# Performance work log

Measured on AMD Instinct MI355X. Metric: run time of the kernel, lower is better.

Reference implementation:

```python
import jax, jax.numpy as jnp
import numpy as np

K = 32          # neighbors
EPS = 1e-8


def _knn_gather(x, k):
    """x: [B,N,3] -> neighbors [B,N,k,3] via cdist + top-k (irregular gather)."""
    sq = jnp.sum(x * x, axis=-1)                                   # [B,N]
    # squared pairwise distances  [B,N,N]
    d = sq[:, :, None] + sq[:, None, :] - 2.0 * jnp.einsum('bnd,bmd->bnm', x, x)
    _, idx = jax.lax.top_k(-d, k)                                  # [B,N,k] nearest (incl. self)
    nbrs = jax.vmap(lambda pts, ind: pts[ind])(x, idx)             # [B,N,k,3]
    return nbrs


def _gpc2(x, k, lv):
    """Geometric point grouping: per-point 15 (or 30 with LV) channel features."""
    nbrs = _knn_gather(x, k)                                       # [B,N,k,3]
    rel = nbrs - x[:, :, None, :]                                  # relative offsets
    mu = jnp.mean(rel, axis=2)                                     # Laplace vector [B,N,3]
    r_max = jnp.max(rel, axis=2)
    r_min = jnp.min(rel, axis=2)
    r_std = jnp.std(rel, axis=2)
    feats = [x, mu, r_max, r_min, r_std]
    if lv:
        unit_mu = mu / (jnp.linalg.norm(mu, axis=-1, keepdims=True) + EPS)
        feats += [x - mu,
                  unit_mu,
                  jnp.cross(x, unit_mu),
                  jnp.max(rel * rel, axis=2),
                  jnp.mean(rel * rel, axis=2)]                     # +15 -> 30 channels
    return jnp.concatenate(feats, axis=-1)                         # [B,N,inc]


def setup_inputs() -> dict:
    key = jax.random.key(0)
    kx, kw = jax.random.split(key)
    B, N, emb, inc = 16, 4096, 32, 30
    x = jax.random.normal(kx, (B, N, 3), dtype=jnp.float32)
    W = jax.random.normal(kw, (emb, inc), dtype=jnp.float32) * 0.1
    b = jnp.zeros((emb,), dtype=jnp.float32)
    return {"x": x, "W": W, "b": b}


def reference(x, W, b):
    in_f = _gpc2(x, K, lv=True)                                    # [B,N,30]
    pooled = jnp.max(in_f, axis=1)                                 # [B,30] global max-pool
    return pooled @ W.T + b                                        # [B,32]
```

## Files before the change

### kernel.cpp

```cpp
#include <hip/hip_runtime.h>

#pragma clang fp contract(off)

#define BATCH 16
#define NPTS  4096
#define KNN   32
#define CH    30
#define NW    8
#define CHUNK (NPTS / NW)
#define FD    30
#define FSTR  31

#define INF_F __builtin_inff()

__device__ __forceinline__ unsigned enc_f32(float f) {
    unsigned u = __float_as_uint(f);
    return (u & 0x80000000u) ? ~u : (u | 0x80000000u);
}
__device__ __forceinline__ float dec_f32(unsigned e) {
    unsigned u = (e & 0x80000000u) ? (e & 0x7FFFFFFFu) : ~e;
    return __uint_as_float(u);
}

__device__ __forceinline__ float med3f(float a, float b, float c) {
#if __has_builtin(__builtin_amdgcn_fmed3f)
    return __builtin_amdgcn_fmed3f(a, b, c);
#else
    float r;
    asm("v_med3_f32 %0, %1, %2, %3" : "=v"(r) : "v"(a), "v"(b), "v"(c));
    return r;
#endif
}

__device__ __forceinline__ float dist3d(float qx, float qy, float qz,
                                        float px, float py, float pz) {
    float r0 = px - qx, r1 = py - qy, r2 = pz - qz;
    return __builtin_fmaf(r0, r0, __builtin_fmaf(r1, r1, r2 * r2));
}

__global__ void init_pool_kernel(unsigned* __restrict__ pool) {
    int i = blockIdx.x * blockDim.x + threadIdx.x;
    if (i < BATCH * CH) pool[i] = 0u;
}

__launch_bounds__(512, 8)
__global__ void knn_kernel(const float* __restrict__ x,
                           unsigned* __restrict__ pool) {
    __shared__ unsigned short fifo[NW * 64 * FSTR];
    __shared__ float scratch[CH * 64];
    __shared__ unsigned char cbs[NW * 64];

    const int b   = blockIdx.x >> 6;
    const int qg  = blockIdx.x & 63;
    const int tid = threadIdx.x;
    const int w   = tid >> 6;
    const int l   = tid & 63;
    const int q   = qg * 64 + l;
    const float* __restrict__ xb = x + (size_t)b * NPTS * 3;

    const float qx = xb[q * 3 + 0], qy = xb[q * 3 + 1], qz = xb[q * 3 + 2];

    const int wu = __builtin_amdgcn_readfirstlane(w);
    const float* __restrict__ cw = xb + (size_t)wu * (CHUNK * 3);

    float B0 = INF_F, B1 = INF_F, B2 = INF_F, B3 = INF_F;
#define INSERT4(dv)                          \
    {                                        \
        B3 = med3f(B2, B3, (dv));            \
        B2 = med3f(B1, B2, (dv));            \
        B1 = med3f(B0, B1, (dv));            \
        B0 = fminf(B0, (dv));                \
    }
#pragma unroll 4
    for (int m = 0; m < CHUNK; ++m) {
        float px = cw[3 * m + 0], py = cw[3 * m + 1], pz = cw[3 * m + 2];
        float d = dist3d(qx, qy, qz, px, py, pz);
        INSERT4(d);
    }
#undef INSERT4
    scratch[w * 64 + l] = B3;
    __syncthreads();
    float t_cap = scratch[l];
#pragma unroll
    for (int ww = 1; ww < NW; ++ww) t_cap = fmaxf(t_cap, scratch[ww * 64 + l]);

    unsigned short* __restrict__ fl = fifo + (w * 64 + l) * FSTR;
    int cnt = 0;
#pragma unroll 4
    for (int m = 0; m < CHUNK; ++m) {
        float px = cw[3 * m + 0], py = cw[3 * m + 1], pz = cw[3 * m + 2];
        float d = dist3d(qx, qy, qz, px, py, pz);
        bool t = (d <= t_cap) && (cnt < FD);
        fl[t ? cnt : FD] = (unsigned short)(wu * CHUNK + m);
        cnt += t;
    }
    cbs[w * 64 + l] = (unsigned char)cnt;
    __syncthreads();

    float* __restrict__ feat = scratch;

#define BSTEP(V, K, J)                                            \
    {                                                             \
        float pv_ = __shfl_xor((V), (J), 64);                     \
        bool km_ = (((l & (K)) == 0) == ((l & (J)) == 0));        \
        (V) = km_ ? fminf((V), pv_) : fmaxf((V), pv_);            \
    }
#define SORT64(V)                                                      \
    BSTEP(V, 2, 1)                                                     \
    BSTEP(V, 4, 2)  BSTEP(V, 4, 1)                                     \
    BSTEP(V, 8, 4)  BSTEP(V, 8, 2)  BSTEP(V, 8, 1)                     \
    BSTEP(V, 16, 8) BSTEP(V, 16, 4) BSTEP(V, 16, 2) BSTEP(V, 16, 1)    \
    BSTEP(V, 32,16) BSTEP(V, 32, 8) BSTEP(V, 32, 4) BSTEP(V, 32, 2) BSTEP(V, 32, 1) \
    BSTEP(V, 64,32) BSTEP(V, 64,16) BSTEP(V, 64, 8) BSTEP(V, 64, 4) BSTEP(V, 64, 2) BSTEP(V, 64, 1)
#define CLEAN64(V) \
    BSTEP(V, 64,32) BSTEP(V, 64,16) BSTEP(V, 64, 8) BSTEP(V, 64, 4) BSTEP(V, 64, 2) BSTEP(V, 64, 1)

#define SURV_LOAD(OFF, DOR, PX, PY, PZ)                                       \
    {                                                                         \
        int o_ = (OFF) + l;                                                   \
        int base_ = 0;                                                        \
        base_ = (o_ >= P1) ? P1 : base_;  base_ = (o_ >= P2) ? P2 : base_;    \
        base_ = (o_ >= P3) ? P3 : base_;  base_ = (o_ >= P4) ? P4 : base_;    \
        base_ = (o_ >= P5) ? P5 : base_;  base_ = (o_ >= P6) ? P6 : base_;    \
        base_ = (o_ >= P7) ? P7 : base_;                                      \
        int reg_ = (o_>=P1)+(o_>=P2)+(o_>=P3)+(o_>=P4)+(o_>=P5)+(o_>=P6)+(o_>=P7); \
        int s_ = o_ - base_;  s_ = (s_ > FD) ? FD : s_;                       \
        int idx_ = (int)fifo[(reg_ * 64 + j) * FSTR + s_];                    \
        const float* pp_ = xb + 3 * idx_;                                     \
        (PX) = pp_[0]; (PY) = pp_[1]; (PZ) = pp_[2];                          \
        float d_ = dist3d(qjx, qjy, qjz, (PX), (PY), (PZ));                   \
        (DOR) = (o_ < S) ? d_ : INF_F;                                        \
    }

#define RSUM(V) { _Pragma("unroll") for (int o_ = 32; o_ >= 1; o_ >>= 1) (V) += __shfl_xor((V), o_, 64); }
#define RMAXW(V) { _Pragma("unroll") for (int o_ = 32; o_ >= 1; o_ >>= 1) (V) = fmaxf((V), __shfl_xor((V), o_, 64)); }
#define RMINW(V) { _Pragma("unroll") for (int o_ = 32; o_ >= 1; o_ >>= 1) (V) = fminf((V), __shfl_xor((V), o_, 64)); }

#pragma unroll 1
    for (int jj = 0; jj < 8; ++jj) {
        const int j  = w * 8 + jj;
        const int qj = qg * 64 + j;
        const float qjx = xb[qj * 3 + 0], qjy = xb[qj * 3 + 1], qjz = xb[qj * 3 + 2];

        const int c0 = cbs[0 * 64 + j], c1 = cbs[1 * 64 + j],
                  c2 = cbs[2 * 64 + j], c3 = cbs[3 * 64 + j],
                  c4 = cbs[4 * 64 + j], c5 = cbs[5 * 64 + j],
                  c6 = cbs[6 * 64 + j], c7 = cbs[7 * 64 + j];
        const int P1 = c0,      P2 = P1 + c1, P3 = P2 + c2, P4 = P3 + c3,
                  P5 = P4 + c4, P6 = P5 + c5, P7 = P6 + c6, S  = P7 + c7;

        float px1, py1, pz1, dor1;
        SURV_LOAD(0, dor1, px1, py1, pz1);
        float v = dor1;
        SORT64(v)

        float thr;
        float px2 = 0.f, py2 = 0.f, pz2 = 0.f, dor2 = INF_F;
        const bool two = (S > 64);
        if (two) {
            SURV_LOAD(64, dor2, px2, py2, pz2);
            float v2 = dor2;
            SORT64(v2)
            float rb = __shfl(v2, 63 - l, 64);
            float lo = fminf(v, rb);
            CLEAN64(lo)
            thr = __shfl(lo, 31, 64);
        } else {
            thr = __shfl(v, 31, 64);
        }

        const unsigned long long blt = (l == 0) ? 0ull : (~0ull >> (64 - l));
        unsigned long long meq1 = __ballot(dor1 == thr);
        int clt = __popcll(__ballot(dor1 < thr));
        int neq1 = __popcll(meq1);
        int rank1 = __popcll(meq1 & blt);
        int rank2 = 0;
        if (two) {
            unsigned long long meq2 = __ballot(dor2 == thr);
            clt += __popcll(__ballot(dor2 < thr));
            rank2 = neq1 + __popcll(meq2 & blt);
        }
        const int need = KNN - clt;
        const bool take1 = (dor1 < thr) || ((dor1 == thr) && (rank1 < need));
        const bool take2 = two && ((dor2 < thr) || ((dor2 == thr) && (rank2 < need)));

        float r10 = px1 - qjx, r11 = py1 - qjy, r12 = pz1 - qjz;
        float r20 = px2 - qjx, r21 = py2 - qjy, r22 = pz2 - qjz;
        float s0 = (take1 ? r10 : 0.f) + (take2 ? r20 : 0.f);
        float s1 = (take1 ? r11 : 0.f) + (take2 ? r21 : 0.f);
        float s2 = (take1 ? r12 : 0.f) + (take2 ? r22 : 0.f);
        float ss0 = (take1 ? r10 * r10 : 0.f) + (take2 ? r20 * r20 : 0.f);
        float ss1 = (take1 ? r11 * r11 : 0.f) + (take2 ? r21 * r21 : 0.f);
        float ss2 = (take1 ? r12 * r12 : 0.f) + (take2 ? r22 * r22 : 0.f);
        float mx0 = fmaxf(take1 ? r10 : -INF_F, take2 ? r20 : -INF_F);
        float mx1 = fmaxf(take1 ? r11 : -INF_F, take2 ? r21 : -INF_F);
        float mx2 = fmaxf(take1 ? r12 : -INF_F, take2 ? r22 : -INF_F);
        float mn0 = fminf(take1 ? r10 : INF_F, take2 ? r20 : INF_F);
        float mn1 = fminf(take1 ? r11 : INF_F, take2 ? r21 : INF_F);
        float mn2 = fminf(take1 ? r12 : INF_F, take2 ? r22 : INF_F);

        RSUM(s0)  RSUM(s1)  RSUM(s2)
        RSUM(ss0) RSUM(ss1) RSUM(ss2)
        RMAXW(mx0) RMAXW(mx1) RMAXW(mx2)
        RMINW(mn0) RMINW(mn1) RMINW(mn2)

        const float invk = 1.0f / (float)KNN;
        float mu0 = s0 * invk, mu1 = s1 * invk, mu2 = s2 * invk;
        float ex0 = ss0 * invk, ex1 = ss1 * invk, ex2 = ss2 * invk;
        float st0 = sqrtf(fmaxf(ex0 - mu0 * mu0, 0.f));
        float st1 = sqrtf(fmaxf(ex1 - mu1 * mu1, 0.f));
        float st2 = sqrtf(fmaxf(ex2 - mu2 * mu2, 0.f));
        float nrm = sqrtf(mu0 * mu0 + mu1 * mu1 + mu2 * mu2) + 1e-8f;
        float u0 = mu0 / nrm, u1 = mu1 / nrm, u2 = mu2 / nrm;
        float cr0 = qjy * u2 - qjz * u1;
        float cr1 = qjz * u0 - qjx * u2;
        float cr2 = qjx * u1 - qjy * u0;
        float mq0 = fmaxf(mx0 * mx0, mn0 * mn0);
        float mq1 = fmaxf(mx1 * mx1, mn1 * mn1);
        float mq2 = fmaxf(mx2 * mx2, mn2 * mn2);

        if (l == 0) {
            feat[ 0 * 64 + j] = qjx;        feat[ 1 * 64 + j] = qjy;
            feat[ 2 * 64 + j] = qjz;        feat[ 3 * 64 + j] = mu0;
            feat[ 4 * 64 + j] = mu1;        feat[ 5 * 64 + j] = mu2;
            feat[ 6 * 64 + j] = mx0;        feat[ 7 * 64 + j] = mx1;
            feat[ 8 * 64 + j] = mx2;        feat[ 9 * 64 + j] = mn0;
            feat[10 * 64 + j] = mn1;        feat[11 * 64 + j] = mn2;
            feat[12 * 64 + j] = st0;        feat[13 * 64 + j] = st1;
            feat[14 * 64 + j] = st2;        feat[15 * 64 + j] = qjx - mu0;
            feat[16 * 64 + j] = qjy - mu1;  feat[17 * 64 + j] = qjz - mu2;
            feat[18 * 64 + j] = u0;         feat[19 * 64 + j] = u1;
            feat[20 * 64 + j] = u2;         feat[21 * 64 + j] = cr0;
            feat[22 * 64 + j] = cr1;        feat[23 * 64 + j] = cr2;
            feat[24 * 64 + j] = mq0;        feat[25 * 64 + j] = mq1;
            feat[26 * 64 + j] = mq2;        feat[27 * 64 + j] = ex0;
            feat[28 * 64 + j] = ex1;        feat[29 * 64 + j] = ex2;
        }
    }
    __syncthreads();

    if (w == 0) {
        for (int c = 0; c < CH; ++c) {
            float v_ = feat[c * 64 + l];
            RMAXW(v_)
            if (l == 0) atomicMax(pool + b * CH + c, enc_f32(v_));
        }
    }
#undef BSTEP
#undef SORT64
#undef CLEAN64
#undef SURV_LOAD
#undef RSUM
#undef RMAXW
#undef RMINW
}

__global__ void final_mm_kernel(const unsigned* __restrict__ pool,
                                const float* __restrict__ W,
                                const float* __restrict__ bias,
                                float* __restrict__ out) {
    int t = blockIdx.x * blockDim.x + threadIdx.x;
    if (t >= BATCH * 32) return;
    int bb = t >> 5, e = t & 31;
    float acc = bias[e];
#pragma unroll
    for (int c = 0; c < CH; ++c)
        acc += dec_f32(pool[bb * CH + c]) * W[e * CH + c];
    out[bb * 32 + e] = acc;
}

extern "C" void kernel_launch(void* const* d_in, const int* in_sizes, int n_in,
                              void* d_out, int out_size, void* d_ws, size_t ws_size,
                              hipStream_t stream) {
    const float* x    = (const float*)d_in[0];
    const float* W    = (const float*)d_in[1];
    const float* bias = (const float*)d_in[2];
    float*       out  = (float*)d_out;
    unsigned*    pool = (unsigned*)d_ws;

    hipLaunchKernelGGL(init_pool_kernel, dim3(1), dim3(512), 0, stream, pool);
    hipLaunchKernelGGL(knn_kernel, dim3(BATCH * (NPTS / 64)), dim3(512),
                       0, stream, x, pool);
    hipLaunchKernelGGL(final_mm_kernel, dim3(1), dim3(512), 0, stream, pool, W, bias, out);
}
```

Measured before the change: 203.7 us.

## Stage candidate points through LDS in two halves for KNN scans

Each block now copies its batch's points into shared memory in two 2048-point halves with float4 loads, and both the top-4 threshold pass and the candidate-collection pass read from LDS instead of global memory. Each wave now scans a strided slice of every half rather than one contiguous chunk, with a larger unroll. The goal is to replace repeated uniform global/scalar loads with LDS reads. In exchange it adds 24KB of LDS per block, extra barriers, and lowers the launch-bounds occupancy hint to 2 blocks.

```diff
diff --git a/kernel.cpp b/kernel.cpp
--- a/kernel.cpp
+++ b/kernel.cpp
@@ -7,7 +7,8 @@
 #define KNN   32
 #define CH    30
 #define NW    8
-#define CHUNK (NPTS / NW)
+#define HALF  2048
+#define HCH   (HALF / NW)
 #define FD    30
 #define FSTR  31
 
@@ -43,9 +44,10 @@
     if (i < BATCH * CH) pool[i] = 0u;
 }
 
-__launch_bounds__(512, 8)
+__launch_bounds__(512, 2)
 __global__ void knn_kernel(const float* __restrict__ x,
                            unsigned* __restrict__ pool) {
+    __shared__ float pts[HALF * 3];
     __shared__ unsigned short fifo[NW * 64 * FSTR];
     __shared__ float scratch[CH * 64];
     __shared__ unsigned char cbs[NW * 64];
@@ -60,8 +62,14 @@
 
     const float qx = xb[q * 3 + 0], qy = xb[q * 3 + 1], qz = xb[q * 3 + 2];
 
-    const int wu = __builtin_amdgcn_readfirstlane(w);
-    const float* __restrict__ cw = xb + (size_t)wu * (CHUNK * 3);
+#define STAGE(h)                                                      \
+    {                                                                 \
+        const float4* __restrict__ src_ = (const float4*)(xb + (h) * (HALF * 3)); \
+        float4* __restrict__ dst_ = (float4*)pts;                     \
+        _Pragma("unroll")                                             \
+        for (int i_ = 0; i_ < 3; ++i_)                                \
+            dst_[tid + i_ * 512] = src_[tid + i_ * 512];              \
+    }
 
     float B0 = INF_F, B1 = INF_F, B2 = INF_F, B3 = INF_F;
 #define INSERT4(dv)                          \
@@ -71,13 +79,21 @@
         B1 = med3f(B0, B1, (dv));            \
         B0 = fminf(B0, (dv));                \
     }
-#pragma unroll 4
-    for (int m = 0; m < CHUNK; ++m) {
-        float px = cw[3 * m + 0], py = cw[3 * m + 1], pz = cw[3 * m + 2];
-        float d = dist3d(qx, qy, qz, px, py, pz);
-        INSERT4(d);
+#pragma unroll 1
+    for (int h = 0; h < 2; ++h) {
+        __syncthreads();
+        STAGE(h);
+        __syncthreads();
+        const float* __restrict__ cw = pts + w * (HCH * 3);
+#pragma unroll 16
+        for (int m = 0; m < HCH; ++m) {
+            float px = cw[3 * m + 0], py = cw[3 * m + 1], pz = cw[3 * m + 2];
+            float d = dist3d(qx, qy, qz, px, py, pz);
+            INSERT4(d);
+        }
     }
 #undef INSERT4
+    __syncthreads();
     scratch[w * 64 + l] = B3;
     __syncthreads();
     float t_cap = scratch[l];
@@ -86,13 +102,21 @@
 
     unsigned short* __restrict__ fl = fifo + (w * 64 + l) * FSTR;
     int cnt = 0;
-#pragma unroll 4
-    for (int m = 0; m < CHUNK; ++m) {
-        float px = cw[3 * m + 0], py = cw[3 * m + 1], pz = cw[3 * m + 2];
-        float d = dist3d(qx, qy, qz, px, py, pz);
-        bool t = (d <= t_cap) && (cnt < FD);
-        fl[t ? cnt : FD] = (unsigned short)(wu * CHUNK + m);
-        cnt += t;
+#pragma unroll 1
+    for (int h = 0; h < 2; ++h) {
+        __syncthreads();
+        STAGE(h);
+        __syncthreads();
+        const float* __restrict__ cw = pts + w * (HCH * 3);
+        const int gbase = h * HALF + w * HCH;
+#pragma unroll 16
+        for (int m = 0; m < HCH; ++m) {
+            float px = cw[3 * m + 0], py = cw[3 * m + 1], pz = cw[3 * m + 2];
+            float d = dist3d(qx, qy, qz, px, py, pz);
+            bool t = (d <= t_cap) && (cnt < FD);
+            fl[t ? cnt : FD] = (unsigned short)(gbase + m);
+            cnt += t;
+        }
     }
     cbs[w * 64 + l] = (unsigned char)cnt;
     __syncthreads();
@@ -253,6 +277,7 @@
 #undef RSUM
 #undef RMAXW
 #undef RMINW
+#undef STAGE
 }
 
 __global__ void final_mm_kernel(const unsigned* __restrict__ pool,
```

New measurement: 243.3 us. +19.4%, slower.

## Process two queries per lane with packed distance math and LDS atomic pooling

Applied to the files above, without the earlier changes.

Each block now handles 128 queries, and every lane keeps two independent top-4 candidate sets. Each candidate point loaded from global memory is reused for two queries, and the distance computation uses 2-wide float vectors. The per-block feature staging plus wave max-reduction is replaced by LDS atomicMax into a 30-entry pool, followed by one global atomic per channel. The per-query FIFO depth drops to 28, which may raise overflow handling. Launch bounds drop to 4 blocks per SM and the grid is halved, trading occupancy for more independent work per lane.

```diff
diff --git a/kernel.cpp b/kernel.cpp
--- a/kernel.cpp
+++ b/kernel.cpp
@@ -8,10 +8,13 @@
 #define CH    30
 #define NW    8
 #define CHUNK (NPTS / NW)
-#define FD    30
-#define FSTR  31
+#define QPB   128
+#define FD    28
+#define FSTR  29
 
 #define INF_F __builtin_inff()
+
+typedef __attribute__((ext_vector_type(2))) float f32x2;
 
 __device__ __forceinline__ unsigned enc_f32(float f) {
     unsigned u = __float_as_uint(f);
@@ -38,66 +41,80 @@
     return __builtin_fmaf(r0, r0, __builtin_fmaf(r1, r1, r2 * r2));
 }
 
+__device__ __forceinline__ f32x2 dist2q(f32x2 qxx, f32x2 qyy, f32x2 qzz,
+                                        float px, float py, float pz) {
+    f32x2 r0 = px - qxx, r1 = py - qyy, r2 = pz - qzz;
+    return __builtin_elementwise_fma(r0, r0,
+           __builtin_elementwise_fma(r1, r1, r2 * r2));
+}
+
 __global__ void init_pool_kernel(unsigned* __restrict__ pool) {
     int i = blockIdx.x * blockDim.x + threadIdx.x;
     if (i < BATCH * CH) pool[i] = 0u;
 }
 
-__launch_bounds__(512, 8)
+__launch_bounds__(512, 4)
 __global__ void knn_kernel(const float* __restrict__ x,
                            unsigned* __restrict__ pool) {
-    __shared__ unsigned short fifo[NW * 64 * FSTR];
-    __shared__ float scratch[CH * 64];
-    __shared__ unsigned char cbs[NW * 64];
-
-    const int b   = blockIdx.x >> 6;
-    const int qg  = blockIdx.x & 63;
+    __shared__ unsigned short fifo[NW * QPB * FSTR];
+    __shared__ float t8[NW * QPB];
+    __shared__ unsigned char cbs[NW * QPB];
+    __shared__ unsigned pool_lds[CH];
+
+    const int b   = blockIdx.x >> 5;
+    const int g   = blockIdx.x & 31;
     const int tid = threadIdx.x;
     const int w   = tid >> 6;
     const int l   = tid & 63;
-    const int q   = qg * 64 + l;
     const float* __restrict__ xb = x + (size_t)b * NPTS * 3;
 
-    const float qx = xb[q * 3 + 0], qy = xb[q * 3 + 1], qz = xb[q * 3 + 2];
+    if (tid < CH) pool_lds[tid] = 0u;
+
+    const int qA = g * QPB + l;
+    const int qB = qA + 64;
+    const f32x2 qxx = { xb[qA * 3 + 0], xb[qB * 3 + 0] };
+    const f32x2 qyy = { xb[qA * 3 + 1], xb[qB * 3 + 1] };
+    const f32x2 qzz = { xb[qA * 3 + 2], xb[qB * 3 + 2] };
 
     const int wu = __builtin_amdgcn_readfirstlane(w);
     const float* __restrict__ cw = xb + (size_t)wu * (CHUNK * 3);
 
-    float B0 = INF_F, B1 = INF_F, B2 = INF_F, B3 = INF_F;
-#define INSERT4(dv)                          \
-    {                                        \
-        B3 = med3f(B2, B3, (dv));            \
-        B2 = med3f(B1, B2, (dv));            \
-        B1 = med3f(B0, B1, (dv));            \
-        B0 = fminf(B0, (dv));                \
-    }
+    float A0 = INF_F, A1 = INF_F, A2 = INF_F, A3 = INF_F;
+    float C0 = INF_F, C1 = INF_F, C2 = INF_F, C3 = INF_F;
 #pragma unroll 4
     for (int m = 0; m < CHUNK; ++m) {
         float px = cw[3 * m + 0], py = cw[3 * m + 1], pz = cw[3 * m + 2];
-        float d = dist3d(qx, qy, qz, px, py, pz);
-        INSERT4(d);
-    }
-#undef INSERT4
-    scratch[w * 64 + l] = B3;
+        f32x2 dd = dist2q(qxx, qyy, qzz, px, py, pz);
+        float dA = dd[0], dB = dd[1];
+        A3 = med3f(A2, A3, dA); A2 = med3f(A1, A2, dA);
+        A1 = med3f(A0, A1, dA); A0 = fminf(A0, dA);
+        C3 = med3f(C2, C3, dB); C2 = med3f(C1, C2, dB);
+        C1 = med3f(C0, C1, dB); C0 = fminf(C0, dB);
+    }
+    t8[w * QPB + l]      = A3;
+    t8[w * QPB + 64 + l] = C3;
     __syncthreads();
-    float t_cap = scratch[l];
+    float tcA = t8[l], tcB = t8[64 + l];
 #pragma unroll
-    for (int ww = 1; ww < NW; ++ww) t_cap = fmaxf(t_cap, scratch[ww * 64 + l]);
-
-    unsigned short* __restrict__ fl = fifo + (w * 64 + l) * FSTR;
-    int cnt = 0;
+    for (int ww = 1; ww < NW; ++ww) {
+        tcA = fmaxf(tcA, t8[ww * QPB + l]);
+        tcB = fmaxf(tcB, t8[ww * QPB + 64 + l]);
+    }
+
+    unsigned short* __restrict__ fA = fifo + (w * QPB + l) * FSTR;
+    unsigned short* __restrict__ fB = fifo + (w * QPB + 64 + l) * FSTR;
+    int cntA = 0, cntB = 0;
 #pragma unroll 4
     for (int m = 0; m < CHUNK; ++m) {
         float px = cw[3 * m + 0], py = cw[3 * m + 1], pz = cw[3 * m + 2];
-        float d = dist3d(qx, qy, qz, px, py, pz);
-        bool t = (d <= t_cap) && (cnt < FD);
-        fl[t ? cnt : FD] = (unsigned short)(wu * CHUNK + m);
-        cnt += t;
-    }
-    cbs[w * 64 + l] = (unsigned char)cnt;
+        f32x2 dd = dist2q(qxx, qyy, qzz, px, py, pz);
+        unsigned short gi = (unsigned short)(wu * CHUNK + m);
+        { bool t = (dd[0] <= tcA) && (cntA < FD); fA[t ? cntA : FD] = gi; cntA += t; }
+        { bool t = (dd[1] <= tcB) && (cntB < FD); fB[t ? cntB : FD] = gi; cntB += t; }
+    }
+    cbs[w * QPB + l]      = (unsigned char)cntA;
+    cbs[w * QPB + 64 + l] = (unsigned char)cntB;
     __syncthreads();
-
-    float* __restrict__ feat = scratch;
 
 #define BSTEP(V, K, J)                                            \
     {                                                             \
@@ -125,7 +142,7 @@
         base_ = (o_ >= P7) ? P7 : base_;                                      \
         int reg_ = (o_>=P1)+(o_>=P2)+(o_>=P3)+(o_>=P4)+(o_>=P5)+(o_>=P6)+(o_>=P7); \
         int s_ = o_ - base_;  s_ = (s_ > FD) ? FD : s_;                       \
-        int idx_ = (int)fifo[(reg_ * 64 + j) * FSTR + s_];                    \
+        int idx_ = (int)fifo[(reg_ * QPB + j) * FSTR + s_];                   \
         const float* pp_ = xb + 3 * idx_;                                     \
         (PX) = pp_[0]; (PY) = pp_[1]; (PZ) = pp_[2];                          \
         float d_ = dist3d(qjx, qjy, qjz, (PX), (PY), (PZ));                   \
@@ -137,15 +154,15 @@
 #define RMINW(V) { _Pragma("unroll") for (int o_ = 32; o_ >= 1; o_ >>= 1) (V) = fminf((V), __shfl_xor((V), o_, 64)); }
 
 #pragma unroll 1
-    for (int jj = 0; jj < 8; ++jj) {
-        const int j  = w * 8 + jj;
-        const int qj = qg * 64 + j;
+    for (int jj = 0; jj < 16; ++jj) {
+        const int j  = w * 16 + jj;
+        const int qj = g * QPB + j;
         const float qjx = xb[qj * 3 + 0], qjy = xb[qj * 3 + 1], qjz = xb[qj * 3 + 2];
 
-        const int c0 = cbs[0 * 64 + j], c1 = cbs[1 * 64 + j],
-                  c2 = cbs[2 * 64 + j], c3 = cbs[3 * 64 + j],
-                  c4 = cbs[4 * 64 + j], c5 = cbs[5 * 64 + j],
-                  c6 = cbs[6 * 64 + j], c7 = cbs[7 * 64 + j];
+        const int c0 = cbs[0 * QPB + j], c1 = cbs[1 * QPB + j],
+                  c2 = cbs[2 * QPB + j], c3 = cbs[3 * QPB + j],
+                  c4 = cbs[4 * QPB + j], c5 = cbs[5 * QPB + j],
+                  c6 = cbs[6 * QPB + j], c7 = cbs[7 * QPB + j];
         const int P1 = c0,      P2 = P1 + c1, P3 = P2 + c2, P4 = P3 + c3,
                   P5 = P4 + c4, P6 = P5 + c5, P7 = P6 + c6, S  = P7 + c7;
 
@@ -220,32 +237,42 @@
         float mq2 = fmaxf(mx2 * mx2, mn2 * mn2);
 
         if (l == 0) {
-            feat[ 0 * 64 + j] = qjx;        feat[ 1 * 64 + j] = qjy;
-            feat[ 2 * 64 + j] = qjz;        feat[ 3 * 64 + j] = mu0;
-            feat[ 4 * 64 + j] = mu1;        feat[ 5 * 64 + j] = mu2;
-            feat[ 6 * 64 + j] = mx0;        feat[ 7 * 64 + j] = mx1;
-            feat[ 8 * 64 + j] = mx2;        feat[ 9 * 64 + j] = mn0;
-            feat[10 * 64 + j] = mn1;        feat[11 * 64 + j] = mn2;
-            feat[12 * 64 + j] = st0;        feat[13 * 64 + j] = st1;
-            feat[14 * 64 + j] = st2;        feat[15 * 64 + j] = qjx - mu0;
-            feat[16 * 64 + j] = qjy - mu1;  feat[17 * 64 + j] = qjz - mu2;
-            feat[18 * 64 + j] = u0;         feat[19 * 64 + j] = u1;
-            feat[20 * 64 + j] = u2;         feat[21 * 64 + j] = cr0;
-            feat[22 * 64 + j] = cr1;        feat[23 * 64 + j] = cr2;
-            feat[24 * 64 + j] = mq0;        feat[25 * 64 + j] = mq1;
-            feat[26 * 64 + j] = mq2;        feat[27 * 64 + j] = ex0;
-            feat[28 * 64 + j] = ex1;        feat[29 * 64 + j] = ex2;
+            atomicMax(&pool_lds[ 0], enc_f32(qjx));
+            atomicMax(&pool_lds[ 1], enc_f32(qjy));
+            atomicMax(&pool_lds[ 2], enc_f32(qjz));
+            atomicMax(&pool_lds[ 3], enc_f32(mu0));
+            atomicMax(&pool_lds[ 4], enc_f32(mu1));
+            atomicMax(&pool_lds[ 5], enc_f32(mu2));
+            atomicMax(&pool_lds[ 6], enc_f32(mx0));
+            atomicMax(&pool_lds[ 7], enc_f32(mx1));
+            atomicMax(&pool_lds[ 8], enc_f32(mx2));
+            atomicMax(&pool_lds[ 9], enc_f32(mn0));
+            atomicMax(&pool_lds[10], enc_f32(mn1));
+            atomicMax(&pool_lds[11], enc_f32(mn2));
+            atomicMax(&pool_lds[12], enc_f32(st0));
+            atomicMax(&pool_lds[13], enc_f32(st1));
+            atomicMax(&pool_lds[14], enc_f32(st2));
+            atomicMax(&pool_lds[15], enc_f32(qjx - mu0));
+            atomicMax(&pool_lds[16], enc_f32(qjy - mu1));
+            atomicMax(&pool_lds[17], enc_f32(qjz - mu2));
+            atomicMax(&pool_lds[18], enc_f32(u0));
+            atomicMax(&pool_lds[19], enc_f32(u1));
+            atomicMax(&pool_lds[20], enc_f32(u2));
+            atomicMax(&pool_lds[21], enc_f32(cr0));
+            atomicMax(&pool_lds[22], enc_f32(cr1));
+            atomicMax(&pool_lds[23], enc_f32(cr2));
+            atomicMax(&pool_lds[24], enc_f32(mq0));
+            atomicMax(&pool_lds[25], enc_f32(mq1));
+            atomicMax(&pool_lds[26], enc_f32(mq2));
+            atomicMax(&pool_lds[27], enc_f32(ex0));
+            atomicMax(&pool_lds[28], enc_f32(ex1));
+            atomicMax(&pool_lds[29], enc_f32(ex2));
         }
     }
     __syncthreads();
 
-    if (w == 0) {
-        for (int c = 0; c < CH; ++c) {
-            float v_ = feat[c * 64 + l];
-            RMAXW(v_)
-            if (l == 0) atomicMax(pool + b * CH + c, enc_f32(v_));
-        }
-    }
+    if (tid < CH)
+        atomicMax(pool + b * CH + tid, pool_lds[tid]);
 #undef BSTEP
 #undef SORT64
 #undef CLEAN64
@@ -279,7 +306,7 @@
     unsigned*    pool = (unsigned*)d_ws;
 
     hipLaunchKernelGGL(init_pool_kernel, dim3(1), dim3(512), 0, stream, pool);
-    hipLaunchKernelGGL(knn_kernel, dim3(BATCH * (NPTS / 64)), dim3(512),
+    hipLaunchKernelGGL(knn_kernel, dim3(BATCH * (NPTS / QPB)), dim3(512),
                        0, stream, x, pool);
     hipLaunchKernelGGL(final_mm_kernel, dim3(1), dim3(512), 0, stream, pool, W, bias, out);
 }
```

After: 270.5 us. 32.8% more time.
